# Performance work log

Measured on AMD Instinct MI355X. Metric: run time of the kernel, lower is better.

## Reference

```python
import jax, jax.numpy as jnp
import numpy as np
from jax import lax

M = 4  # signature truncation level (matches init kwarg m)


def setup_inputs() -> dict:
    key = jax.random.key(0)
    x = jax.random.normal(key, (2048, 256, 10), dtype=jnp.float32)
    return {"x": x}


def _signature(x, m):
    """Truncated path signature via Chen's identity.

    x: (B, L, d) path. Returns (B, sum_{k=1..m} d^k), levels 1..m concatenated
    in row-major tensor order (matching iisignature.sig layout).
    Recurrence: S <- S \otimes exp(dx_t), where exp(v) has level-k term v^{\otimes k}/k!.
    """
    B, L, d = x.shape
    dx = x[:, 1:, :] - x[:, :-1, :]  # (B, L-1, d) path increments

    def step(carry, v):
        # carry: tuple of (B, d^k) signature levels; v: (B, d) increment
        # segment signature: seg[k] = v^{\otimes(k+1)} / (k+1)!
        seg = [v]
        for k in range(1, m):
            seg.append((seg[-1][:, :, None] * v[:, None, :]).reshape(B, -1) / (k + 1))
        # truncated tensor-algebra product: new_k = S_k + seg_k + sum_i S_i (x) seg_{k-1-i}
        new = []
        for k in range(m):
            t = carry[k] + seg[k]
            for i in range(k):
                t = t + (carry[i][:, :, None] * seg[k - 1 - i][:, None, :]).reshape(B, -1)
            new.append(t)
        return tuple(new), None

    init = tuple(jnp.zeros((B, d ** (k + 1)), x.dtype) for k in range(m))
    final, _ = lax.scan(step, init, jnp.moveaxis(dx, 1, 0))
    return jnp.concatenate(final, axis=-1)


def reference(x):
    return _signature(x, M)
```

## Files before the change

kernel.cpp:

```cpp
#include <hip/hip_runtime.h>


#define SIG 11110

typedef short bf16x8 __attribute__((ext_vector_type(8)));
typedef float f32x4  __attribute__((ext_vector_type(4)));

__device__ __forceinline__ unsigned cvt_pk2(float lo, float hi) {
    unsigned r;
    asm("v_cvt_pk_bf16_f32 %0, %1, %2" : "=v"(r) : "v"(lo), "v"(hi));
    return r;
}
__device__ __forceinline__ unsigned split_pack(float a) {
    const float hi = __uint_as_float(__float_as_uint(a) & 0xFFFF0000u);
    return cvt_pk2(hi, a - hi);
}

template<int MI, int NI>
__device__ __forceinline__ void consume(const unsigned* __restrict__ Pb,
                                        const unsigned* __restrict__ Qb,
                                        int r0, int c0, int lane,
                                        f32x4 (&acc)[MI][NI]) {
    const int slot = lane >> 4, rr = lane & 15;
    bf16x8 Bf[NI];
    #pragma unroll
    for (int ni = 0; ni < NI; ++ni)
        Bf[ni] = *(const bf16x8*)(Qb + slot * 448 + (c0 + ni * 16 + rr) * 4);
    #pragma unroll
    for (int mi = 0; mi < MI; ++mi) {
        const bf16x8 Af = *(const bf16x8*)(Pb + slot * 448 + (r0 + mi * 16 + rr) * 4);
        #pragma unroll
        for (int ni = 0; ni < NI; ++ni)
            acc[mi][ni] = __builtin_amdgcn_mfma_f32_16x16x32_bf16(Af, Bf[ni], acc[mi][ni], 0, 0, 0);
    }
}

template<int MI, int NI>
__device__ __forceinline__ void write_seg(int r0, int c0, int lane,
                                          const f32x4 (&acc)[MI][NI],
                                          float* __restrict__ out, size_t base) {
    #pragma unroll
    for (int mi = 0; mi < MI; ++mi) {
        #pragma unroll
        for (int ni = 0; ni < NI; ++ni) {
            #pragma unroll
            for (int r = 0; r < 4; ++r) {
                const int m = r0 + mi * 16 + (lane >> 4) * 4 + r;
                const int n = c0 + ni * 16 + (lane & 15);
                if (m < 100) {
                    if (n < 100)      out[base + 1110 + m * 100 + n]         = acc[mi][ni][r];
                    else if (n < 110) out[base + 110  + m * 10  + (n - 100)] = acc[mi][ni][r];
                }
            }
        }
    }
}

template<int NV>
__device__ __forceinline__ void produce_t(int ch, const float* __restrict__ xs,
                                          unsigned* __restrict__ Pb,
                                          unsigned* __restrict__ Qb,
                                          bool isPair, bool isCell, bool isVcol,
                                          int tid, int qrow, int i1, int i2,
                                          float x0i, float xL2,
                                          float& c1, float& c2, float& Ds) {
    if (isPair) {
        unsigned q0 = 0, q1 = 0;
        #pragma unroll
        for (int tl = 0; tl < 8; ++tl) {
            unsigned pa, pr;
            if (tl < NV) {
                const float n1 = xs[(ch * 8 + tl + 1) * 10 + i1];
                const float n2 = xs[(ch * 8 + tl + 1) * 10 + i2];
                const float vi = n1 - c1, vj = n2 - c2;
                const float s1f = c1 - x0i;
                const float r1  = vi * vj;
                const float r2  = s1f * vj;
                const float a   = fmaf(r1, 1.f/6.f, fmaf(r2, 0.5f, Ds));
                pa = split_pack(a);
                pr = cvt_pk2(r1, r2);
                Ds += fmaf(0.5f, r1, r2);
                c1 = n1; c2 = n2;
            } else { pa = 0u; pr = 0u; }
            if ((tl & 1) == 0) { q0 = pa; q1 = pr; }
            else *(uint4*)&Pb[(tl >> 1) * 448 + tid * 4] = make_uint4(q0, q1, pa, pr);
        }
    } else if (isCell) {
        unsigned q0 = 0, q1 = 0;
        #pragma unroll
        for (int tl = 0; tl < 8; ++tl) {
            unsigned pu, pw;
            if (tl < NV) {
                const float n1 = xs[(ch * 8 + tl + 1) * 10 + i1];
                const float n2 = xs[(ch * 8 + tl + 1) * 10 + i2];
                const float vk = n1 - c1, vl = n2 - c2;
                const float w  = vk * vl;
                const float m2 = fmaf(-0.5f, c2 + n2, xL2);
                const float uw = vk * m2;
                pu = cvt_pk2(uw, uw);
                pw = cvt_pk2(w * (-1.f/24.f), w * (-1.f/12.f));
                c1 = n1; c2 = n2;
            } else { pu = 0u; pw = 0u; }
            if ((tl & 1) == 0) { q0 = pu; q1 = pw; }
            else *(uint4*)&Qb[(tl >> 1) * 448 + qrow * 4] = make_uint4(q0, q1, pu, pw);
        }
    } else if (isVcol) {
        unsigned q0 = 0;
        #pragma unroll
        for (int tl = 0; tl < 8; ++tl) {
            unsigned pv;
            if (tl < NV) {
                const float n1 = xs[(ch * 8 + tl + 1) * 10 + i1];
                pv = cvt_pk2(n1 - c1, n1 - c1);
                c1 = n1;
            } else pv = 0u;
            if ((tl & 1) == 0) q0 = pv;
            else *(uint4*)&Qb[(tl >> 1) * 448 + qrow * 4] = make_uint4(q0, 0u, pv, 0u);
        }
    }
}

template<int MIA, int NIA, int R0A, int C0A, int MIB, int NIB, int R0B, int C0B>
__device__ __forceinline__ void run_wave(const float* __restrict__ xs,
                                         unsigned (&Pl)[2][1792],
                                         unsigned (&Ql)[2][1792],
                                         bool isPair, bool isCell, bool isVcol,
                                         int tid, int qrow, int i1, int i2,
                                         float x0i, float xL2, float c1, float c2,
                                         int lane, float* __restrict__ out, size_t base) {
    float Ds = 0.f;
    f32x4 accA[MIA][NIA];
    #pragma unroll
    for (int mi = 0; mi < MIA; ++mi)
        #pragma unroll
        for (int ni = 0; ni < NIA; ++ni) accA[mi][ni] = (f32x4){0.f, 0.f, 0.f, 0.f};
    constexpr int MB = (MIB > 0) ? MIB : 1;
    constexpr int NB = (NIB > 0) ? NIB : 1;
    f32x4 accB[MB][NB];
    if constexpr (MIB > 0) {
        #pragma unroll
        for (int mi = 0; mi < MB; ++mi)
            #pragma unroll
            for (int ni = 0; ni < NB; ++ni) accB[mi][ni] = (f32x4){0.f, 0.f, 0.f, 0.f};
    }

    produce_t<8>(0, xs, Pl[0], Ql[0], isPair, isCell, isVcol,
                 tid, qrow, i1, i2, x0i, xL2, c1, c2, Ds);
    __syncthreads();

    for (int ch = 0; ch < 32; ++ch) {
        const unsigned* Pb = Pl[ch & 1];
        const unsigned* Qb = Ql[ch & 1];
        consume<MIA, NIA>(Pb, Qb, R0A, C0A, lane, accA);
        if constexpr (MIB > 0) consume<MIB, NIB>(Pb, Qb, R0B, C0B, lane, accB);
        if (ch < 30)
            produce_t<8>(ch + 1, xs, Pl[(ch + 1) & 1], Ql[(ch + 1) & 1],
                         isPair, isCell, isVcol, tid, qrow, i1, i2, x0i, xL2, c1, c2, Ds);
        else if (ch == 30)
            produce_t<7>(31, xs, Pl[1], Ql[1],
                         isPair, isCell, isVcol, tid, qrow, i1, i2, x0i, xL2, c1, c2, Ds);
        __syncthreads();
    }

    if (isPair) out[base + 10 + tid] = Ds;
    write_seg<MIA, NIA>(R0A, C0A, lane, accA, out, base);
    if constexpr (MIB > 0) write_seg<MIB, NIB>(R0B, C0B, lane, accB, out, base);
}

__global__ __launch_bounds__(256, 4)
void sig_mfma14(const float* __restrict__ xg, float* __restrict__ out) {
    __shared__ float    xs[2560];
    __shared__ unsigned Pl[2][1792];
    __shared__ unsigned Ql[2][1792];

    const int tid  = threadIdx.x;
    const int b    = blockIdx.x;
    const int lane = tid & 63;
    const int wv   = tid >> 6;
    const float* __restrict__ xb = xg + (size_t)b * 2560;

    #pragma unroll
    for (int r = 0; r < 10; ++r) xs[r * 256 + tid] = xb[r * 256 + tid];
    for (int e = tid; e < 384; e += 256) {
        const int buf = e / 192, r = e % 192, slot = r / 48, rem = r % 48;
        Pl[buf][slot * 448 + (100 + rem / 4) * 4 + (rem & 3)] = 0u;
    }
    if (tid < 64) {
        const int buf = tid / 32, r = tid % 32, slot = r / 8, rem = r % 8;
        Ql[buf][slot * 448 + (110 + rem / 4) * 4 + (rem & 3)] = 0u;
    }
    __syncthreads();

    const bool isPair = (tid < 100);
    const int  qrow   = tid - 128;
    const bool isCell = (qrow >= 0) && (qrow < 100);
    const bool isVcol = (qrow >= 100) && (qrow < 110);

    int i1 = 0, i2 = 0;
    if (isPair)      { i1 = tid / 10;  i2 = tid - i1 * 10; }
    else if (isCell) { i1 = qrow / 10; i2 = qrow - i1 * 10; }
    else if (isVcol) { i1 = qrow - 100; i2 = i1; }

    const float c1 = xs[i1], c2 = xs[i2];
    const float x0i = c1;
    const float xL2 = xs[2550 + i2];
    const size_t base = (size_t)b * SIG;

    if      (wv == 0) run_wave<4, 3,  0,  0, 0, 0, 0,  0>(xs, Pl, Ql, isPair, isCell, isVcol,
                          tid, qrow, i1, i2, x0i, xL2, c1, c2, lane, out, base);
    else if (wv == 1) run_wave<3, 3, 64,  0, 4, 1, 0, 96>(xs, Pl, Ql, isPair, isCell, isVcol,
                          tid, qrow, i1, i2, x0i, xL2, c1, c2, lane, out, base);
    else if (wv == 2) run_wave<4, 3,  0, 48, 0, 0, 0,  0>(xs, Pl, Ql, isPair, isCell, isVcol,
                          tid, qrow, i1, i2, x0i, xL2, c1, c2, lane, out, base);
    else              run_wave<3, 4, 64, 48, 0, 0, 0,  0>(xs, Pl, Ql, isPair, isCell, isVcol,
                          tid, qrow, i1, i2, x0i, xL2, c1, c2, lane, out, base);

    if (tid < 10) out[base + tid] = xs[2550 + tid] - xs[tid];
}

extern "C" void kernel_launch(void* const* d_in, const int* in_sizes, int n_in,
                              void* d_out, int out_size, void* d_ws, size_t ws_size,
                              hipStream_t stream) {
    const float* x = (const float*)d_in[0];
    float* out = (float*)d_out;
    const int B = in_sizes[0] / 2560;
    sig_mfma14<<<B, 256, 0, stream>>>(x, out);
}
```

Before: 91.79 us.

## Precompute transposed path increments in LDS and vectorize producer loads

The kernel now stores path increments in LDS as a dimension-major transposed array (padded stride 260) instead of raw positions. Producers read eight increments per chunk with float4 loads, carry running sums instead of previous positions, and no longer need a special 7-step final chunk because the padding entry is zero. It also swaps which thread groups build the pair and cell operands and reassigns the MFMA output tiles across the four waves. The aim is to cut scalar LDS reads and per-step subtraction in the producer and to rebalance wave work, at the cost of a strided transpose during setup.

```diff
diff --git a/kernel.cpp b/kernel.cpp
--- a/kernel.cpp
+++ b/kernel.cpp
@@ -56,64 +56,60 @@
     }
 }
 
-template<int NV>
-__device__ __forceinline__ void produce_t(int ch, const float* __restrict__ xs,
-                                          unsigned* __restrict__ Pb,
-                                          unsigned* __restrict__ Qb,
-                                          bool isPair, bool isCell, bool isVcol,
-                                          int tid, int qrow, int i1, int i2,
-                                          float x0i, float xL2,
-                                          float& c1, float& c2, float& Ds) {
+__device__ __forceinline__ void produce(int ch, const float* __restrict__ vt,
+                                        unsigned* __restrict__ Pb,
+                                        unsigned* __restrict__ Qb,
+                                        bool isPair, bool isCell, bool isVcol,
+                                        int prow, int qrow, int i1, int i2,
+                                        float& s1f, float& Rv, float& Ds) {
     if (isPair) {
+        const float4 a0 = *(const float4*)(vt + i1 * 260 + ch * 8);
+        const float4 a1 = *(const float4*)(vt + i1 * 260 + ch * 8 + 4);
+        const float4 b0 = *(const float4*)(vt + i2 * 260 + ch * 8);
+        const float4 b1 = *(const float4*)(vt + i2 * 260 + ch * 8 + 4);
+        const float v1[8] = {a0.x,a0.y,a0.z,a0.w,a1.x,a1.y,a1.z,a1.w};
+        const float v2[8] = {b0.x,b0.y,b0.z,b0.w,b1.x,b1.y,b1.z,b1.w};
         unsigned q0 = 0, q1 = 0;
         #pragma unroll
         for (int tl = 0; tl < 8; ++tl) {
-            unsigned pa, pr;
-            if (tl < NV) {
-                const float n1 = xs[(ch * 8 + tl + 1) * 10 + i1];
-                const float n2 = xs[(ch * 8 + tl + 1) * 10 + i2];
-                const float vi = n1 - c1, vj = n2 - c2;
-                const float s1f = c1 - x0i;
-                const float r1  = vi * vj;
-                const float r2  = s1f * vj;
-                const float a   = fmaf(r1, 1.f/6.f, fmaf(r2, 0.5f, Ds));
-                pa = split_pack(a);
-                pr = cvt_pk2(r1, r2);
-                Ds += fmaf(0.5f, r1, r2);
-                c1 = n1; c2 = n2;
-            } else { pa = 0u; pr = 0u; }
+            const float vi = v1[tl], vj = v2[tl];
+            const float r1 = vi * vj;
+            const float r2 = s1f * vj;
+            const float a  = fmaf(r1, 1.f/6.f, fmaf(r2, 0.5f, Ds));
+            const unsigned pa = split_pack(a), pr = cvt_pk2(r1, r2);
+            Ds += fmaf(0.5f, r1, r2);
+            s1f += vi;
             if ((tl & 1) == 0) { q0 = pa; q1 = pr; }
-            else *(uint4*)&Pb[(tl >> 1) * 448 + tid * 4] = make_uint4(q0, q1, pa, pr);
+            else *(uint4*)&Pb[(tl >> 1) * 448 + prow * 4] = make_uint4(q0, q1, pa, pr);
         }
     } else if (isCell) {
+        const float4 a0 = *(const float4*)(vt + i1 * 260 + ch * 8);
+        const float4 a1 = *(const float4*)(vt + i1 * 260 + ch * 8 + 4);
+        const float4 b0 = *(const float4*)(vt + i2 * 260 + ch * 8);
+        const float4 b1 = *(const float4*)(vt + i2 * 260 + ch * 8 + 4);
+        const float v1[8] = {a0.x,a0.y,a0.z,a0.w,a1.x,a1.y,a1.z,a1.w};
+        const float v2[8] = {b0.x,b0.y,b0.z,b0.w,b1.x,b1.y,b1.z,b1.w};
         unsigned q0 = 0, q1 = 0;
         #pragma unroll
         for (int tl = 0; tl < 8; ++tl) {
-            unsigned pu, pw;
-            if (tl < NV) {
-                const float n1 = xs[(ch * 8 + tl + 1) * 10 + i1];
-                const float n2 = xs[(ch * 8 + tl + 1) * 10 + i2];
-                const float vk = n1 - c1, vl = n2 - c2;
-                const float w  = vk * vl;
-                const float m2 = fmaf(-0.5f, c2 + n2, xL2);
-                const float uw = vk * m2;
-                pu = cvt_pk2(uw, uw);
-                pw = cvt_pk2(w * (-1.f/24.f), w * (-1.f/12.f));
-                c1 = n1; c2 = n2;
-            } else { pu = 0u; pw = 0u; }
+            const float vk = v1[tl], vl = v2[tl];
+            const float w  = vk * vl;
+            const float m2 = fmaf(-0.5f, vl, Rv);
+            Rv -= vl;
+            const float uw = vk * m2;
+            const unsigned pu = cvt_pk2(uw, uw);
+            const unsigned pw = cvt_pk2(w * (-1.f/24.f), w * (-1.f/12.f));
             if ((tl & 1) == 0) { q0 = pu; q1 = pw; }
             else *(uint4*)&Qb[(tl >> 1) * 448 + qrow * 4] = make_uint4(q0, q1, pu, pw);
         }
     } else if (isVcol) {
+        const float4 a0 = *(const float4*)(vt + i1 * 260 + ch * 8);
+        const float4 a1 = *(const float4*)(vt + i1 * 260 + ch * 8 + 4);
+        const float v1[8] = {a0.x,a0.y,a0.z,a0.w,a1.x,a1.y,a1.z,a1.w};
         unsigned q0 = 0;
         #pragma unroll
         for (int tl = 0; tl < 8; ++tl) {
-            unsigned pv;
-            if (tl < NV) {
-                const float n1 = xs[(ch * 8 + tl + 1) * 10 + i1];
-                pv = cvt_pk2(n1 - c1, n1 - c1);
-                c1 = n1;
-            } else pv = 0u;
+            const unsigned pv = cvt_pk2(v1[tl], v1[tl]);
             if ((tl & 1) == 0) q0 = pv;
             else *(uint4*)&Qb[(tl >> 1) * 448 + qrow * 4] = make_uint4(q0, 0u, pv, 0u);
         }
@@ -121,12 +117,12 @@
 }
 
 template<int MIA, int NIA, int R0A, int C0A, int MIB, int NIB, int R0B, int C0B>
-__device__ __forceinline__ void run_wave(const float* __restrict__ xs,
+__device__ __forceinline__ void run_wave(const float* __restrict__ vt,
                                          unsigned (&Pl)[2][1792],
                                          unsigned (&Ql)[2][1792],
                                          bool isPair, bool isCell, bool isVcol,
-                                         int tid, int qrow, int i1, int i2,
-                                         float x0i, float xL2, float c1, float c2,
+                                         int prow, int qrow, int i1, int i2,
+                                         float s1f, float Rv,
                                          int lane, float* __restrict__ out, size_t base) {
     float Ds = 0.f;
     f32x4 accA[MIA][NIA];
@@ -144,8 +140,7 @@
             for (int ni = 0; ni < NB; ++ni) accB[mi][ni] = (f32x4){0.f, 0.f, 0.f, 0.f};
     }
 
-    produce_t<8>(0, xs, Pl[0], Ql[0], isPair, isCell, isVcol,
-                 tid, qrow, i1, i2, x0i, xL2, c1, c2, Ds);
+    produce(0, vt, Pl[0], Ql[0], isPair, isCell, isVcol, prow, qrow, i1, i2, s1f, Rv, Ds);
     __syncthreads();
 
     for (int ch = 0; ch < 32; ++ch) {
@@ -153,23 +148,20 @@
         const unsigned* Qb = Ql[ch & 1];
         consume<MIA, NIA>(Pb, Qb, R0A, C0A, lane, accA);
         if constexpr (MIB > 0) consume<MIB, NIB>(Pb, Qb, R0B, C0B, lane, accB);
-        if (ch < 30)
-            produce_t<8>(ch + 1, xs, Pl[(ch + 1) & 1], Ql[(ch + 1) & 1],
-                         isPair, isCell, isVcol, tid, qrow, i1, i2, x0i, xL2, c1, c2, Ds);
-        else if (ch == 30)
-            produce_t<7>(31, xs, Pl[1], Ql[1],
-                         isPair, isCell, isVcol, tid, qrow, i1, i2, x0i, xL2, c1, c2, Ds);
+        if (ch < 31)
+            produce(ch + 1, vt, Pl[(ch + 1) & 1], Ql[(ch + 1) & 1],
+                    isPair, isCell, isVcol, prow, qrow, i1, i2, s1f, Rv, Ds);
         __syncthreads();
     }
 
-    if (isPair) out[base + 10 + tid] = Ds;
+    if (isPair) out[base + 10 + prow] = Ds;
     write_seg<MIA, NIA>(R0A, C0A, lane, accA, out, base);
     if constexpr (MIB > 0) write_seg<MIB, NIB>(R0B, C0B, lane, accB, out, base);
 }
 
 __global__ __launch_bounds__(256, 4)
-void sig_mfma14(const float* __restrict__ xg, float* __restrict__ out) {
-    __shared__ float    xs[2560];
+void sig_mfma15(const float* __restrict__ xg, float* __restrict__ out) {
+    __shared__ float    vt[2600];
     __shared__ unsigned Pl[2][1792];
     __shared__ unsigned Ql[2][1792];
 
@@ -179,8 +171,11 @@
     const int wv   = tid >> 6;
     const float* __restrict__ xb = xg + (size_t)b * 2560;
 
-    #pragma unroll
-    for (int r = 0; r < 10; ++r) xs[r * 256 + tid] = xb[r * 256 + tid];
+    for (int e = tid; e < 2550; e += 256) {
+        const int t = e / 10, d = e - t * 10;
+        vt[d * 260 + t] = xb[e + 10] - xb[e];
+    }
+    if (tid < 10) vt[tid * 260 + 255] = 0.f;
     for (int e = tid; e < 384; e += 256) {
         const int buf = e / 192, r = e % 192, slot = r / 48, rem = r % 48;
         Pl[buf][slot * 448 + (100 + rem / 4) * 4 + (rem & 3)] = 0u;
@@ -191,31 +186,32 @@
     }
     __syncthreads();
 
-    const bool isPair = (tid < 100);
-    const int  qrow   = tid - 128;
-    const bool isCell = (qrow >= 0) && (qrow < 100);
-    const bool isVcol = (qrow >= 100) && (qrow < 110);
+    const int  pid    = tid - 128;
+    const bool isPair = (pid >= 0) && (pid < 100);
+    const bool isCell = (tid < 100);
+    const bool isVcol = (tid >= 100) && (tid < 110);
+    const int  prow   = isPair ? pid : 0;
+    const int  qrow   = tid;
 
     int i1 = 0, i2 = 0;
-    if (isPair)      { i1 = tid / 10;  i2 = tid - i1 * 10; }
-    else if (isCell) { i1 = qrow / 10; i2 = qrow - i1 * 10; }
-    else if (isVcol) { i1 = qrow - 100; i2 = i1; }
-
-    const float c1 = xs[i1], c2 = xs[i2];
-    const float x0i = c1;
-    const float xL2 = xs[2550 + i2];
+    if (isPair)      { i1 = pid / 10; i2 = pid - i1 * 10; }
+    else if (isCell) { i1 = tid / 10; i2 = tid - i1 * 10; }
+    else if (isVcol) { i1 = tid - 100; i2 = i1; }
+
+    const float s1f = 0.f;
+    const float Rv  = isCell ? (xb[2550 + i2] - xb[i2]) : 0.f;
     const size_t base = (size_t)b * SIG;
 
-    if      (wv == 0) run_wave<4, 3,  0,  0, 0, 0, 0,  0>(xs, Pl, Ql, isPair, isCell, isVcol,
-                          tid, qrow, i1, i2, x0i, xL2, c1, c2, lane, out, base);
-    else if (wv == 1) run_wave<3, 3, 64,  0, 4, 1, 0, 96>(xs, Pl, Ql, isPair, isCell, isVcol,
-                          tid, qrow, i1, i2, x0i, xL2, c1, c2, lane, out, base);
-    else if (wv == 2) run_wave<4, 3,  0, 48, 0, 0, 0,  0>(xs, Pl, Ql, isPair, isCell, isVcol,
-                          tid, qrow, i1, i2, x0i, xL2, c1, c2, lane, out, base);
-    else              run_wave<3, 4, 64, 48, 0, 0, 0,  0>(xs, Pl, Ql, isPair, isCell, isVcol,
-                          tid, qrow, i1, i2, x0i, xL2, c1, c2, lane, out, base);
-
-    if (tid < 10) out[base + tid] = xs[2550 + tid] - xs[tid];
+    if      (wv == 0) run_wave<4, 3,  0, 48, 0, 0,  0,  0>(vt, Pl, Ql, isPair, isCell, isVcol,
+                          prow, qrow, i1, i2, s1f, Rv, lane, out, base);
+    else if (wv == 1) run_wave<3, 3, 64, 48, 4, 1,  0, 96>(vt, Pl, Ql, isPair, isCell, isVcol,
+                          prow, qrow, i1, i2, s1f, Rv, lane, out, base);
+    else if (wv == 2) run_wave<4, 3,  0,  0, 0, 0,  0,  0>(vt, Pl, Ql, isPair, isCell, isVcol,
+                          prow, qrow, i1, i2, s1f, Rv, lane, out, base);
+    else              run_wave<3, 3, 64,  0, 3, 1, 64, 96>(vt, Pl, Ql, isPair, isCell, isVcol,
+                          prow, qrow, i1, i2, s1f, Rv, lane, out, base);
+
+    if (tid < 10) out[base + tid] = xb[2550 + tid] - xb[tid];
 }
 
 extern "C" void kernel_launch(void* const* d_in, const int* in_sizes, int n_in,
@@ -224,5 +220,5 @@
     const float* x = (const float*)d_in[0];
     float* out = (float*)d_out;
     const int B = in_sizes[0] / 2560;
-    sig_mfma14<<<B, 256, 0, stream>>>(x, out);
-}
+    sig_mfma15<<<B, 256, 0, stream>>>(x, out);
+}
```

Measured after the change: 86.20 us. 6.1% less time.
